# Optimization experiments

Measured on AMD Instinct MI355X. Metric: run time of the kernel, lower is better.

## Reference

```python
import jax, jax.numpy as jnp
import numpy as np

B, N, D = 8, 4096, 1024
NC, NU = 8, 32            # core / universal experts (num_experts=16, occ_factor=1/4)
E = NC + NU               # 40 total experts
S = 2                     # slots per expert
HC, HU = 4 * D, D         # core hidden = 4*dim, occ hidden = 4*occ_factor*dim = dim
L2_EPS = 1e-6
LN_EPS = 1e-5


def l2norm(x):
    n = jnp.sqrt(jnp.sum(x * x, axis=-1, keepdims=True))
    return x * (1.0 / (n + L2_EPS))


def layernorm(x, g, b):
    mu = jnp.mean(x, axis=-1, keepdims=True)
    var = jnp.mean((x - mu) ** 2, axis=-1, keepdims=True)
    return (x - mu) / jnp.sqrt(var + LN_EPS) * g + b


def entmax15(z):
    # exact 1.5-entmax over last axis (sorted algorithm, Peters et al. 2019)
    z = z / 2.0
    z = z - jnp.max(z, axis=-1, keepdims=True)
    zs = -jnp.sort(-z, axis=-1)                      # descending
    K = z.shape[-1]
    k = jnp.arange(1, K + 1, dtype=z.dtype)
    mean = jnp.cumsum(zs, axis=-1) / k
    meansq = jnp.cumsum(zs * zs, axis=-1) / k
    ss = k * (meansq - mean * mean)
    delta = jnp.maximum((1.0 - ss) / k, 1e-12)
    tau = mean - jnp.sqrt(delta)
    support = jnp.sum((tau <= zs).astype(jnp.int32), axis=-1, keepdims=True)
    tau_star = jnp.take_along_axis(tau, support - 1, axis=-1)
    return jnp.maximum(z - tau_star, 0.0) ** 2


def setup_inputs() -> dict:
    key = jax.random.key(0)
    ks = jax.random.split(key, 8)
    return {
        "x": jax.random.normal(ks[0], (B, N, D), jnp.float32),
        "attn_weight": jax.random.uniform(ks[1], (B, 128), jnp.float32),
        "phi": jax.random.normal(ks[2], (E, S, D), jnp.float32) * 0.02,
        "key_gamma": jnp.ones((D,), jnp.float32),
        "key_beta": jnp.zeros((D,), jnp.float32),
        "query_gamma": jnp.ones((D,), jnp.float32),
        "query_beta": jnp.zeros((D,), jnp.float32),
        "ln_gamma": jnp.ones((D,), jnp.float32),
        "ln_beta": jnp.zeros((D,), jnp.float32),
        "scale0": jnp.asarray(0.5, jnp.float32),
        "scale1": jnp.asarray(0.5, jnp.float32),
        "core_w1": jax.random.normal(ks[3], (NC, D, HC), jnp.float32) * (D ** -0.5),
        "core_b1": jnp.zeros((NC, HC), jnp.float32),
        "core_w2": jax.random.normal(ks[4], (NC, HC, D), jnp.float32) * (HC ** -0.5),
        "core_b2": jnp.zeros((NC, D), jnp.float32),
        "occ_w1": jax.random.normal(ks[5], (NU, D, HU), jnp.float32) * (D ** -0.5),
        "occ_b1": jnp.zeros((NU, HU), jnp.float32),
        "occ_w2": jax.random.normal(ks[6], (NU, HU, D), jnp.float32) * (HU ** -0.5),
        "occ_b2": jnp.zeros((NU, D), jnp.float32),
    }


def _expert_mlp(s, w1, b1, w2, b2):
    # s: [b, e, s, d]; per-expert 2-layer MLP with exact GELU
    h = jax.nn.gelu(jnp.einsum('besd,edh->besh', s, w1) + b1[None, :, None, :], approximate=False)
    return jnp.einsum('besh,ehd->besd', h, w2) + b2[None, :, None, :]


def reference(x, attn_weight, phi, key_gamma, key_beta, query_gamma, query_beta,
              ln_gamma, ln_beta, scale0, scale1,
              core_w1, core_b1, core_w2, core_b2,
              occ_w1, occ_b1, occ_w2, occ_b2):
    # keys: OffsetScale then l2norm
    k = l2norm(x * key_gamma + key_beta)
    # queries: OffsetScale -> LayerNorm -> l2norm on phi
    q = layernorm(phi * query_gamma + query_beta, ln_gamma, ln_beta)
    q = l2norm(q)
    logits = jnp.einsum('bnd,esd->bnes', k, q)                      # [B,N,E,S]
    core_mask = (jnp.arange(E) < NC)[None, None, :, None]
    adjusted = jnp.where(core_mask, logits, jnp.asarray(-10000.0, logits.dtype))
    dispatch = jax.nn.softmax(adjusted / scale0, axis=2)            # softmax over experts
    combine = entmax15((adjusted / scale1).reshape(B, N, E * S))    # [B,N,E*S]
    slots = jnp.einsum('bnd,bnes->besd', x, dispatch)               # [B,E,S,D]
    core_out = _expert_mlp(slots[:, :NC], core_w1, core_b1, core_w2, core_b2)
    occ_out = _expert_mlp(slots[:, NC:], occ_w1, occ_b1, occ_w2, occ_b2)
    out = jnp.concatenate([core_out, occ_out], axis=1).reshape(B, E * S, D)
    return jnp.einsum('bsd,bns->bnd', out, combine)                 # [B,N,D]
```

## Files before the change

kernel.cpp:

```cpp
#include <hip/hip_runtime.h>
#include <hip/hip_bf16.h>

#define B_ 8
#define N_ 4096
#define D_ 1024

typedef __attribute__((ext_vector_type(8))) short short8_t;
typedef __attribute__((ext_vector_type(4))) float f32x4;

__device__ __forceinline__ unsigned short f2bf(float f) {
    union { float f; unsigned int u; } v; v.f = f;
    unsigned int r = v.u + 0x7FFF + ((v.u >> 16) & 1);
    return (unsigned short)(r >> 16);
}

__global__ __launch_bounds__(64) void k_prep(
    const float* __restrict__ phi, const float* __restrict__ qg, const float* __restrict__ qb,
    const float* __restrict__ lng, const float* __restrict__ lnb,
    const float* __restrict__ kg, const float* __restrict__ kb,
    unsigned short* __restrict__ qkb, float* __restrict__ cj, float* __restrict__ wbuf)
{
    int r = blockIdx.x;
    int lane = threadIdx.x;
    if (r == 16) {
        float cacc = 0.f;
#pragma unroll
        for (int c = 0; c < 16; ++c) {
            int i = c * 64 + lane;
            float g = kg[i], b = kb[i];
            wbuf[i] = g * g;
            wbuf[1024 + i] = 2.0f * g * b;
            cacc += b * b;
        }
#pragma unroll
        for (int m = 32; m; m >>= 1) cacc += __shfl_xor(cacc, m);
        if (lane == 0) wbuf[2048] = cacc;
        return;
    }
    const float* pr = phi + (size_t)r * D_;
    float v[16];
    float s1 = 0.f;
#pragma unroll
    for (int c = 0; c < 16; ++c) {
        int i = c * 64 + lane;
        v[c] = pr[i] * qg[i] + qb[i];
        s1 += v[c];
    }
#pragma unroll
    for (int m = 32; m; m >>= 1) s1 += __shfl_xor(s1, m);
    float mu = s1 * (1.0f / D_);
    float s2 = 0.f;
#pragma unroll
    for (int c = 0; c < 16; ++c) { float dd = v[c] - mu; s2 += dd * dd; }
#pragma unroll
    for (int m = 32; m; m >>= 1) s2 += __shfl_xor(s2, m);
    float var = s2 * (1.0f / D_);
    float inv = 1.0f / sqrtf(var + 1e-5f);
    float u[16];
    float s3 = 0.f;
#pragma unroll
    for (int c = 0; c < 16; ++c) {
        int i = c * 64 + lane;
        u[c] = (v[c] - mu) * inv * lng[i] + lnb[i];
        s3 += u[c] * u[c];
    }
#pragma unroll
    for (int m = 32; m; m >>= 1) s3 += __shfl_xor(s3, m);
    float rn = 1.0f / (sqrtf(s3) + 1e-6f);
    float cacc = 0.f;
#pragma unroll
    for (int c = 0; c < 16; ++c) {
        int i = c * 64 + lane;
        float qv = u[c] * rn;
        qkb[(size_t)r * D_ + i] = f2bf(qv * kg[i]);
        cacc += qv * kb[i];
    }
#pragma unroll
    for (int m = 32; m; m >>= 1) cacc += __shfl_xor(cacc, m);
    if (lane == 0) cj[r] = cacc;
}

__global__ __launch_bounds__(512) void k_fused(
    const float* __restrict__ x, const unsigned short* __restrict__ qkb,
    const float* __restrict__ wbuf, const float* __restrict__ cj,
    const float* __restrict__ s0p,
    float* __restrict__ lgbuf, float* __restrict__ spart)
{
    __shared__ float smem[6336];
    float* wsd  = smem;
    float* part = smem + 2048;
    float* nrmp = smem + 4096;
    float* sums = smem + 4224;
    float* disp = smem + 5312;

    int tid = threadIdx.x;
    int tok0 = blockIdx.x * 64;
    int wv = tid >> 6;
    int lane = tid & 63;
    int wt = wv & 3;
    int kh = wv >> 2;
    int am = lane & 15;
    int kgr = lane >> 4;

    ((float4*)wsd)[tid] = ((const float4*)wbuf)[tid];
    __syncthreads();

    const float* xrow = x + (size_t)(tok0 + wt * 16 + am) * D_ + kh * 512 + kgr * 8;
    const unsigned short* qrow = qkb + (size_t)am * 1024 + kh * 512 + kgr * 8;
    const float* w2row = wsd + kh * 512 + kgr * 8;
    const float* w1row = wsd + 1024 + kh * 512 + kgr * 8;

    f32x4 acc = {0.f, 0.f, 0.f, 0.f};
    float nrm = 0.f;
#pragma unroll 2
    for (int ks = 0; ks < 16; ++ks) {
        int off = ks * 32;
        float4 a0  = *(const float4*)(xrow + off);
        float4 a1  = *(const float4*)(xrow + off + 4);
        float4 w2a = *(const float4*)(w2row + off);
        float4 w2b = *(const float4*)(w2row + off + 4);
        float4 w1a = *(const float4*)(w1row + off);
        float4 w1b = *(const float4*)(w1row + off + 4);
        nrm += (w2a.x * a0.x + w1a.x) * a0.x + (w2a.y * a0.y + w1a.y) * a0.y
             + (w2a.z * a0.z + w1a.z) * a0.z + (w2a.w * a0.w + w1a.w) * a0.w
             + (w2b.x * a1.x + w1b.x) * a1.x + (w2b.y * a1.y + w1b.y) * a1.y
             + (w2b.z * a1.z + w1b.z) * a1.z + (w2b.w * a1.w + w1b.w) * a1.w;
        union { unsigned short u[8]; short8_t s; } ua;
        ua.u[0] = f2bf(a0.x); ua.u[1] = f2bf(a0.y);
        ua.u[2] = f2bf(a0.z); ua.u[3] = f2bf(a0.w);
        ua.u[4] = f2bf(a1.x); ua.u[5] = f2bf(a1.y);
        ua.u[6] = f2bf(a1.z); ua.u[7] = f2bf(a1.w);
        short8_t bv = *(const short8_t*)(qrow + off);
        acc = __builtin_amdgcn_mfma_f32_16x16x32_bf16(ua.s, bv, acc, 0, 0, 0);
    }
    nrm += __shfl_xor(nrm, 16);
    nrm += __shfl_xor(nrm, 32);

#pragma unroll
    for (int r = 0; r < 4; ++r)
        part[(kh * 64 + wt * 16 + kgr * 4 + r) * 16 + am] = acc[r];
    if (kgr == 0) nrmp[kh * 64 + wt * 16 + am] = nrm;
    __syncthreads();

#pragma unroll
    for (int it = 0; it < 3; ++it) {
        int idx = tid + it * 512;
        if (idx < 1088) {
            int t = idx / 17, v = idx - t * 17;
            float sv = (v < 16) ? (part[t * 16 + v] + part[1024 + t * 16 + v])
                                : (nrmp[t] + nrmp[64 + t]);
            sums[idx] = sv;
            lgbuf[(size_t)(tok0 + t) * 20 + v] = sv;
        }
    }
    __syncthreads();

    if (tid < 64) {
        const float* sp = sums + tid * 17;
        float ss = sp[16] + wbuf[2048];
        float rn = 1.0f / (sqrtf(ss) + 1e-6f);
        float inv0 = 1.0f / s0p[0];
        float lg[16];
#pragma unroll
        for (int j = 0; j < 16; ++j) lg[j] = (sp[j] + cj[j]) * rn;
        float dsp[16];
#pragma unroll
        for (int sl = 0; sl < 2; ++sl) {
            float a[8], m = -1e30f;
#pragma unroll
            for (int ee = 0; ee < 8; ++ee) { a[ee] = lg[2 * ee + sl] * inv0; m = fmaxf(m, a[ee]); }
            float den = 0.f;
#pragma unroll
            for (int ee = 0; ee < 8; ++ee) { a[ee] = expf(a[ee] - m); den += a[ee]; }
            float r = 1.0f / den;
#pragma unroll
            for (int ee = 0; ee < 8; ++ee) dsp[2 * ee + sl] = a[ee] * r;
        }
#pragma unroll
        for (int q4i = 0; q4i < 4; ++q4i)
            *(float4*)(&disp[tid * 16 + q4i * 4]) =
                make_float4(dsp[q4i * 4 + 0], dsp[q4i * 4 + 1], dsp[q4i * 4 + 2], dsp[q4i * 4 + 3]);
    }
    __syncthreads();

    int th = tid >> 8;
    int cix = tid & 255;
    const float* xp = x + (size_t)tok0 * D_ + cix * 4;
    float4 acc2[8];
#pragma unroll
    for (int j = 0; j < 8; ++j) { acc2[j].x = 0.f; acc2[j].y = 0.f; acc2[j].z = 0.f; acc2[j].w = 0.f; }
#pragma unroll 8
    for (int n = 0; n < 64; ++n) {
        float4 xv = *(const float4*)(xp + (size_t)n * D_);
        const float4* q4 = (const float4*)(disp + n * 16 + th * 8);
        float4 s0 = q4[0], s1 = q4[1];
        acc2[0].x += s0.x * xv.x; acc2[0].y += s0.x * xv.y; acc2[0].z += s0.x * xv.z; acc2[0].w += s0.x * xv.w;
        acc2[1].x += s0.y * xv.x; acc2[1].y += s0.y * xv.y; acc2[1].z += s0.y * xv.z; acc2[1].w += s0.y * xv.w;
        acc2[2].x += s0.z * xv.x; acc2[2].y += s0.z * xv.y; acc2[2].z += s0.z * xv.z; acc2[2].w += s0.z * xv.w;
        acc2[3].x += s0.w * xv.x; acc2[3].y += s0.w * xv.y; acc2[3].z += s0.w * xv.z; acc2[3].w += s0.w * xv.w;
        acc2[4].x += s1.x * xv.x; acc2[4].y += s1.x * xv.y; acc2[4].z += s1.x * xv.z; acc2[4].w += s1.x * xv.w;
        acc2[5].x += s1.y * xv.x; acc2[5].y += s1.y * xv.y; acc2[5].z += s1.y * xv.z; acc2[5].w += s1.y * xv.w;
        acc2[6].x += s1.z * xv.x; acc2[6].y += s1.z * xv.y; acc2[6].z += s1.z * xv.z; acc2[6].w += s1.z * xv.w;
        acc2[7].x += s1.w * xv.x; acc2[7].y += s1.w * xv.y; acc2[7].z += s1.w * xv.z; acc2[7].w += s1.w * xv.w;
    }
    float* op = spart + ((size_t)blockIdx.x * 16 + th * 8) * 1024 + cix * 4;
#pragma unroll
    for (int j = 0; j < 8; ++j)
        *(float4*)(op + (size_t)j * 1024) = acc2[j];
}

__global__ __launch_bounds__(64) void k_epi(
    const float* __restrict__ lgbuf, const float* __restrict__ cj,
    const float* __restrict__ wbuf, const float* __restrict__ s1p,
    float* __restrict__ combine)
{
    int tok = blockIdx.x * 64 + threadIdx.x;
    const float* lp = lgbuf + (size_t)tok * 20;
    float s[17];
    float4 q0 = *(const float4*)(lp + 0);
    float4 q1 = *(const float4*)(lp + 4);
    float4 q2 = *(const float4*)(lp + 8);
    float4 q3 = *(const float4*)(lp + 12);
    s[0] = q0.x; s[1] = q0.y; s[2] = q0.z; s[3] = q0.w;
    s[4] = q1.x; s[5] = q1.y; s[6] = q1.z; s[7] = q1.w;
    s[8] = q2.x; s[9] = q2.y; s[10] = q2.z; s[11] = q2.w;
    s[12] = q3.x; s[13] = q3.y; s[14] = q3.z; s[15] = q3.w;
    s[16] = lp[16];

    float ss = s[16] + wbuf[2048];
    float rn = 1.0f / (sqrtf(ss) + 1e-6f);
    float inv1h = 0.5f / s1p[0];
    float lg[16];
#pragma unroll
    for (int j = 0; j < 16; ++j) lg[j] = (s[j] + cj[j]) * rn;

    float z[16], zmax = -1e30f;
#pragma unroll
    for (int j = 0; j < 16; ++j) { z[j] = lg[j] * inv1h; zmax = fmaxf(zmax, z[j]); }
#pragma unroll
    for (int j = 0; j < 16; ++j) z[j] -= zmax;
    float zsr[16];
#pragma unroll
    for (int j = 0; j < 16; ++j) zsr[j] = z[j];
#pragma unroll
    for (int rr = 0; rr < 16; ++rr) {
#pragma unroll
        for (int jj = (rr & 1); jj + 1 < 16; jj += 2) {
            float aa = zsr[jj], bb = zsr[jj + 1];
            zsr[jj] = fmaxf(aa, bb);
            zsr[jj + 1] = fminf(aa, bb);
        }
    }
    float cs = 0.f, css = 0.f, tau_star = 0.f;
#pragma unroll
    for (int kk = 1; kk <= 16; ++kk) {
        cs += zsr[kk - 1];
        css += zsr[kk - 1] * zsr[kk - 1];
        float fk = (float)kk;
        float mean = cs / fk, msq = css / fk;
        float ssv = fk * (msq - mean * mean);
        float delta = fmaxf((1.0f - ssv) / fk, 1e-12f);
        float tau = mean - sqrtf(delta);
        tau_star = (tau <= zsr[kk - 1]) ? tau : tau_star;
    }
    float4* cw = (float4*)(combine + (size_t)tok * 16);
#pragma unroll
    for (int q4i = 0; q4i < 4; ++q4i) {
        float4 cv;
        float t0 = fmaxf(z[q4i * 4 + 0] - tau_star, 0.f);
        float t1 = fmaxf(z[q4i * 4 + 1] - tau_star, 0.f);
        float t2 = fmaxf(z[q4i * 4 + 2] - tau_star, 0.f);
        float t3 = fmaxf(z[q4i * 4 + 3] - tau_star, 0.f);
        cv.x = t0 * t0; cv.y = t1 * t1; cv.z = t2 * t2; cv.w = t3 * t3;
        cw[q4i] = cv;
    }
}

__global__ __launch_bounds__(256) void k_slots_reduce(
    const float* __restrict__ spart, float* __restrict__ slotsT)
{
    int j = blockIdx.x, b = blockIdx.y;
    int tid = threadIdx.x;
    const float* p = spart + ((size_t)(b * 64) * 16 + j) * 1024 + tid * 4;
    float4 s; s.x = 0.f; s.y = 0.f; s.z = 0.f; s.w = 0.f;
#pragma unroll 8
    for (int nc = 0; nc < 64; ++nc) {
        float4 v = *(const float4*)(p + (size_t)nc * 16384);
        s.x += v.x; s.y += v.y; s.z += v.z; s.w += v.w;
    }
    int e = j >> 1, sl = j & 1;
    int t = b * 2 + sl;
    float* o = slotsT + ((size_t)e * 1024 + tid * 4) * 16 + t;
    o[0] = s.x; o[16] = s.y; o[32] = s.z; o[48] = s.w;
}

__global__ __launch_bounds__(256) void k_mlp1(
    const float* __restrict__ w1, const float* __restrict__ slotsT,
    float* __restrict__ p1)
{
    __shared__ float sm[1024];
    int cc = blockIdx.x, ks = blockIdx.y, e = blockIdx.z;
    int tid = threadIdx.x;
    int k0 = ks * 64;
    int col = cc * 1024 + tid * 4;
    ((float4*)sm)[tid] = ((const float4*)(slotsT + ((size_t)e * 1024 + k0) * 16))[tid];
    __syncthreads();

    const float* wp = w1 + (size_t)e * 1024 * 4096 + (size_t)k0 * 4096 + col;
    float4 acc[16];
#pragma unroll
    for (int t = 0; t < 16; ++t) { acc[t].x = 0.f; acc[t].y = 0.f; acc[t].z = 0.f; acc[t].w = 0.f; }
#pragma unroll 8
    for (int kk = 0; kk < 64; ++kk) {
        float4 w = *(const float4*)(wp + (size_t)kk * 4096);
        const float4* q4 = (const float4*)(sm + kk * 16);
        float4 s0 = q4[0], s1 = q4[1], s2 = q4[2], s3 = q4[3];
        acc[0].x  += s0.x * w.x; acc[0].y  += s0.x * w.y; acc[0].z  += s0.x * w.z; acc[0].w  += s0.x * w.w;
        acc[1].x  += s0.y * w.x; acc[1].y  += s0.y * w.y; acc[1].z  += s0.y * w.z; acc[1].w  += s0.y * w.w;
        acc[2].x  += s0.z * w.x; acc[2].y  += s0.z * w.y; acc[2].z  += s0.z * w.z; acc[2].w  += s0.z * w.w;
        acc[3].x  += s0.w * w.x; acc[3].y  += s0.w * w.y; acc[3].z  += s0.w * w.z; acc[3].w  += s0.w * w.w;
        acc[4].x  += s1.x * w.x; acc[4].y  += s1.x * w.y; acc[4].z  += s1.x * w.z; acc[4].w  += s1.x * w.w;
        acc[5].x  += s1.y * w.x; acc[5].y  += s1.y * w.y; acc[5].z  += s1.y * w.z; acc[5].w  += s1.y * w.w;
        acc[6].x  += s1.z * w.x; acc[6].y  += s1.z * w.y; acc[6].z  += s1.z * w.z; acc[6].w  += s1.z * w.w;
        acc[7].x  += s1.w * w.x; acc[7].y  += s1.w * w.y; acc[7].z  += s1.w * w.z; acc[7].w  += s1.w * w.w;
        acc[8].x  += s2.x * w.x; acc[8].y  += s2.x * w.y; acc[8].z  += s2.x * w.z; acc[8].w  += s2.x * w.w;
        acc[9].x  += s2.y * w.x; acc[9].y  += s2.y * w.y; acc[9].z  += s2.y * w.z; acc[9].w  += s2.y * w.w;
        acc[10].x += s2.z * w.x; acc[10].y += s2.z * w.y; acc[10].z += s2.z * w.z; acc[10].w += s2.z * w.w;
        acc[11].x += s2.w * w.x; acc[11].y += s2.w * w.y; acc[11].z += s2.w * w.z; acc[11].w += s2.w * w.w;
        acc[12].x += s3.x * w.x; acc[12].y += s3.x * w.y; acc[12].z += s3.x * w.z; acc[12].w += s3.x * w.w;
        acc[13].x += s3.y * w.x; acc[13].y += s3.y * w.y; acc[13].z += s3.y * w.z; acc[13].w += s3.y * w.w;
        acc[14].x += s3.z * w.x; acc[14].y += s3.z * w.y; acc[14].z += s3.z * w.z; acc[14].w += s3.z * w.w;
        acc[15].x += s3.w * w.x; acc[15].y += s3.w * w.y; acc[15].z += s3.w * w.z; acc[15].w += s3.w * w.w;
    }
    float av0[16], av1[16], av2[16], av3[16];
#pragma unroll
    for (int t = 0; t < 16; ++t) { av0[t] = acc[t].x; av1[t] = acc[t].y; av2[t] = acc[t].z; av3[t] = acc[t].w; }
    float* op = p1 + (((size_t)ks * 8 + e) * 4096 + col) * 16;
#pragma unroll
    for (int q = 0; q < 4; ++q) {
        *(float4*)(op + 0 * 16 + q * 4) = make_float4(av0[q*4+0], av0[q*4+1], av0[q*4+2], av0[q*4+3]);
        *(float4*)(op + 1 * 16 + q * 4) = make_float4(av1[q*4+0], av1[q*4+1], av1[q*4+2], av1[q*4+3]);
        *(float4*)(op + 2 * 16 + q * 4) = make_float4(av2[q*4+0], av2[q*4+1], av2[q*4+2], av2[q*4+3]);
        *(float4*)(op + 3 * 16 + q * 4) = make_float4(av3[q*4+0], av3[q*4+1], av3[q*4+2], av3[q*4+3]);
    }
}

__global__ __launch_bounds__(256) void k_mlp2f(
    const float* __restrict__ w2, const float* __restrict__ p1,
    const float* __restrict__ b1, float* __restrict__ p2)
{
    __shared__ float sm[1024];
    int ks = blockIdx.x, e = blockIdx.y;
    int tid = threadIdx.x;
    int k0 = ks * 64;
    int col = tid * 4;

    {
        int fidx = tid;
        const float* pp = p1 + (size_t)e * 65536 + (size_t)k0 * 16 + fidx * 4;
        float4 s; s.x = 0.f; s.y = 0.f; s.z = 0.f; s.w = 0.f;
#pragma unroll
        for (int ksp = 0; ksp < 16; ++ksp) {
            float4 v = *(const float4*)(pp + (size_t)ksp * 524288);
            s.x += v.x; s.y += v.y; s.z += v.z; s.w += v.w;
        }
        int colh = k0 + (fidx >> 2);
        float bb = b1[(size_t)e * 4096 + colh];
        s.x += bb; s.y += bb; s.z += bb; s.w += bb;
        s.x = 0.5f * s.x * (1.0f + erff(s.x * 0.70710678118654752f));
        s.y = 0.5f * s.y * (1.0f + erff(s.y * 0.70710678118654752f));
        s.z = 0.5f * s.z * (1.0f + erff(s.z * 0.70710678118654752f));
        s.w = 0.5f * s.w * (1.0f + erff(s.w * 0.70710678118654752f));
        *(float4*)(&sm[fidx * 4]) = s;
    }
    __syncthreads();

    const float* wp = w2 + (size_t)e * 4096 * 1024 + (size_t)k0 * 1024 + col;
    float4 acc[16];
#pragma unroll
    for (int t = 0; t < 16; ++t) { acc[t].x = 0.f; acc[t].y = 0.f; acc[t].z = 0.f; acc[t].w = 0.f; }
#pragma unroll 8
    for (int kk = 0; kk < 64; ++kk) {
        float4 w = *(const float4*)(wp + (size_t)kk * 1024);
        const float4* q4 = (const float4*)(sm + kk * 16);
        float4 s0 = q4[0], s1 = q4[1], s2 = q4[2], s3 = q4[3];
        acc[0].x  += s0.x * w.x; acc[0].y  += s0.x * w.y; acc[0].z  += s0.x * w.z; acc[0].w  += s0.x * w.w;
        acc[1].x  += s0.y * w.x; acc[1].y  += s0.y * w.y; acc[1].z  += s0.y * w.z; acc[1].w  += s0.y * w.w;
        acc[2].x  += s0.z * w.x; acc[2].y  += s0.z * w.y; acc[2].z  += s0.z * w.z; acc[2].w  += s0.z * w.w;
        acc[3].x  += s0.w * w.x; acc[3].y  += s0.w * w.y; acc[3].z  += s0.w * w.z; acc[3].w  += s0.w * w.w;
        acc[4].x  += s1.x * w.x; acc[4].y  += s1.x * w.y; acc[4].z  += s1.x * w.z; acc[4].w  += s1.x * w.w;
        acc[5].x  += s1.y * w.x; acc[5].y  += s1.y * w.y; acc[5].z  += s1.y * w.z; acc[5].w  += s1.y * w.w;
        acc[6].x  += s1.z * w.x; acc[6].y  += s1.z * w.y; acc[6].z  += s1.z * w.z; acc[6].w  += s1.z * w.w;
        acc[7].x  += s1.w * w.x; acc[7].y  += s1.w * w.y; acc[7].z  += s1.w * w.z; acc[7].w  += s1.w * w.w;
        acc[8].x  += s2.x * w.x; acc[8].y  += s2.x * w.y; acc[8].z  += s2.x * w.z; acc[8].w  += s2.x * w.w;
        acc[9].x  += s2.y * w.x; acc[9].y  += s2.y * w.y; acc[9].z  += s2.y * w.z; acc[9].w  += s2.y * w.w;
        acc[10].x += s2.z * w.x; acc[10].y += s2.z * w.y; acc[10].z += s2.z * w.z; acc[10].w += s2.z * w.w;
        acc[11].x += s2.w * w.x; acc[11].y += s2.w * w.y; acc[11].z += s2.w * w.z; acc[11].w += s2.w * w.w;
        acc[12].x += s3.x * w.x; acc[12].y += s3.x * w.y; acc[12].z += s3.x * w.z; acc[12].w += s3.x * w.w;
        acc[13].x += s3.y * w.x; acc[13].y += s3.y * w.y; acc[13].z += s3.y * w.z; acc[13].w += s3.y * w.w;
        acc[14].x += s3.z * w.x; acc[14].y += s3.z * w.y; acc[14].z += s3.z * w.z; acc[14].w += s3.z * w.w;
        acc[15].x += s3.w * w.x; acc[15].y += s3.w * w.y; acc[15].z += s3.w * w.z; acc[15].w += s3.w * w.w;
    }
    float av0[16], av1[16], av2[16], av3[16];
#pragma unroll
    for (int t = 0; t < 16; ++t) { av0[t] = acc[t].x; av1[t] = acc[t].y; av2[t] = acc[t].z; av3[t] = acc[t].w; }
    float* op = p2 + (((size_t)ks * 8 + e) * 1024 + col) * 16;
#pragma unroll
    for (int q = 0; q < 4; ++q) {
        *(float4*)(op + 0 * 16 + q * 4) = make_float4(av0[q*4+0], av0[q*4+1], av0[q*4+2], av0[q*4+3]);
        *(float4*)(op + 1 * 16 + q * 4) = make_float4(av1[q*4+0], av1[q*4+1], av1[q*4+2], av1[q*4+3]);
        *(float4*)(op + 2 * 16 + q * 4) = make_float4(av2[q*4+0], av2[q*4+1], av2[q*4+2], av2[q*4+3]);
        *(float4*)(op + 3 * 16 + q * 4) = make_float4(av3[q*4+0], av3[q*4+1], av3[q*4+2], av3[q*4+3]);
    }
}

__global__ __launch_bounds__(256) void k_red2(
    const float* __restrict__ p2, const float* __restrict__ b2,
    float* __restrict__ co)
{
    int idx = blockIdx.x * 256 + threadIdx.x;
    int q = idx & 3, d = (idx >> 2) & 1023, e = idx >> 12;
    const float* p = p2 + ((size_t)e * 1024 + d) * 16 + q * 4;
    float4 s; s.x = 0.f; s.y = 0.f; s.z = 0.f; s.w = 0.f;
#pragma unroll 8
    for (int ks = 0; ks < 64; ++ks) {
        float4 v = *(const float4*)(p + (size_t)ks * 131072);
        s.x += v.x; s.y += v.y; s.z += v.z; s.w += v.w;
    }
    float bb = b2[(size_t)e * 1024 + d];
    float vv[4] = { s.x + bb, s.y + bb, s.z + bb, s.w + bb };
#pragma unroll
    for (int u = 0; u < 4; ++u) {
        int t = q * 4 + u;
        int b = t >> 1, sl = t & 1;
        co[((size_t)b * 16 + e * 2 + sl) * 1024 + d] = vv[u];
    }
}

__global__ __launch_bounds__(256) void k_out(
    const float* __restrict__ co, const float* __restrict__ combine,
    float* __restrict__ out)
{
    __shared__ float sm[1024];
    int b = blockIdx.y, tile = blockIdx.x;
    int tid = threadIdx.x;
    ((float4*)sm)[tid] = ((const float4*)(combine + ((size_t)b * N_ + tile * 64) * 16))[tid];
    float4 cv[16];
#pragma unroll
    for (int j = 0; j < 16; ++j)
        cv[j] = ((const float4*)(co + ((size_t)b * 16 + j) * 1024))[tid];
    __syncthreads();
    float4* ob = (float4*)(out + ((size_t)b * N_ + tile * 64) * 1024) + tid;
#pragma unroll 2
    for (int it = 0; it < 64; ++it) {
        const float* cm = sm + it * 16;
        float4 acc; acc.x = 0.f; acc.y = 0.f; acc.z = 0.f; acc.w = 0.f;
#pragma unroll
        for (int j = 0; j < 16; ++j) {
            float wj = cm[j];
            acc.x += wj * cv[j].x; acc.y += wj * cv[j].y;
            acc.z += wj * cv[j].z; acc.w += wj * cv[j].w;
        }
        ob[(size_t)it * 256] = acc;
    }
}

extern "C" void kernel_launch(void* const* d_in, const int* in_sizes, int n_in,
                              void* d_out, int out_size, void* d_ws, size_t ws_size,
                              hipStream_t stream)
{
    const float* x   = (const float*)d_in[0];
    const float* phi = (const float*)d_in[2];
    const float* kg  = (const float*)d_in[3];
    const float* kb  = (const float*)d_in[4];
    const float* qg  = (const float*)d_in[5];
    const float* qb  = (const float*)d_in[6];
    const float* lng = (const float*)d_in[7];
    const float* lnb = (const float*)d_in[8];
    const float* s0  = (const float*)d_in[9];
    const float* s1  = (const float*)d_in[10];
    const float* w1  = (const float*)d_in[11];
    const float* b1  = (const float*)d_in[12];
    const float* w2  = (const float*)d_in[13];
    const float* b2  = (const float*)d_in[14];

    float* out = (float*)d_out;
    float* ws  = (float*)d_ws;

    unsigned short* qkb = (unsigned short*)ws;
    float* cj       = ws + 8192;
    float* wbuf     = cj + 16;
    float* combine  = wbuf + 2064;
    float* slotsT   = combine + 524288;
    float* co       = slotsT + 131072;
    float* lgbuf    = co + 131072;
    float* arenaA   = lgbuf + 655360;
    float* arenaB   = arenaA + 8388608;
    float* spart    = arenaA;
    float* p1       = arenaA;
    float* p2       = arenaB;

    k_prep        <<<dim3(17),        dim3(64),  0, stream>>>(phi, qg, qb, lng, lnb, kg, kb, qkb, cj, wbuf);
    k_fused       <<<dim3(512),       dim3(512), 0, stream>>>(x, qkb, wbuf, cj, s0, lgbuf, spart);
    k_epi         <<<dim3(512),       dim3(64),  0, stream>>>(lgbuf, cj, wbuf, s1, combine);
    k_slots_reduce<<<dim3(16, 8),     dim3(256), 0, stream>>>(spart, slotsT);
    k_mlp1        <<<dim3(4, 16, 8),  dim3(256), 0, stream>>>(w1, slotsT, p1);
    k_mlp2f       <<<dim3(64, 8),     dim3(256), 0, stream>>>(w2, p1, b1, p2);
    k_red2        <<<dim3(128),       dim3(256), 0, stream>>>(p2, b2, co);
    k_out         <<<dim3(64, 8),     dim3(256), 0, stream>>>(co, combine, out);
}
```

Baseline: 207.1 us.

## Split fused logits/slot kernel into separate logits and slot-accumulation kernels

The fused kernel is split in two. The first computes logits and the dispatch softmax with 256 threads, each wave covering the full K range, which removes the cross-half partial reduction in shared memory. Dispatch weights go to a global buffer, and a second kernel rereads x and dispatch to accumulate slot partials, each thread now holding all 16 slot accumulators. This removes a sync and the split-K reduction, and lowers register and LDS pressure per kernel. The cost is a second full read of x (128 MB) from memory or L2, plus an extra launch.

```diff
diff --git a/kernel.cpp b/kernel.cpp
--- a/kernel.cpp
+++ b/kernel.cpp
@@ -80,40 +80,36 @@
     if (lane == 0) cj[r] = cacc;
 }
 
-__global__ __launch_bounds__(512) void k_fused(
+__global__ __launch_bounds__(256) void k_logits(
     const float* __restrict__ x, const unsigned short* __restrict__ qkb,
     const float* __restrict__ wbuf, const float* __restrict__ cj,
     const float* __restrict__ s0p,
-    float* __restrict__ lgbuf, float* __restrict__ spart)
-{
-    __shared__ float smem[6336];
+    float* __restrict__ lgbuf, float* __restrict__ dispatch)
+{
+    __shared__ float smem[3136];
     float* wsd  = smem;
-    float* part = smem + 2048;
-    float* nrmp = smem + 4096;
-    float* sums = smem + 4224;
-    float* disp = smem + 5312;
+    float* sums = smem + 2048;
 
     int tid = threadIdx.x;
     int tok0 = blockIdx.x * 64;
     int wv = tid >> 6;
     int lane = tid & 63;
-    int wt = wv & 3;
-    int kh = wv >> 2;
     int am = lane & 15;
     int kgr = lane >> 4;
 
     ((float4*)wsd)[tid] = ((const float4*)wbuf)[tid];
+    ((float4*)wsd)[tid + 256] = ((const float4*)wbuf)[tid + 256];
     __syncthreads();
 
-    const float* xrow = x + (size_t)(tok0 + wt * 16 + am) * D_ + kh * 512 + kgr * 8;
-    const unsigned short* qrow = qkb + (size_t)am * 1024 + kh * 512 + kgr * 8;
-    const float* w2row = wsd + kh * 512 + kgr * 8;
-    const float* w1row = wsd + 1024 + kh * 512 + kgr * 8;
+    const float* xrow = x + (size_t)(tok0 + wv * 16 + am) * D_ + kgr * 8;
+    const unsigned short* qrow = qkb + (size_t)am * 1024 + kgr * 8;
+    const float* w2row = wsd + kgr * 8;
+    const float* w1row = wsd + 1024 + kgr * 8;
 
     f32x4 acc = {0.f, 0.f, 0.f, 0.f};
     float nrm = 0.f;
 #pragma unroll 2
-    for (int ks = 0; ks < 16; ++ks) {
+    for (int ks = 0; ks < 32; ++ks) {
         int off = ks * 32;
         float4 a0  = *(const float4*)(xrow + off);
         float4 a1  = *(const float4*)(xrow + off + 4);
@@ -138,22 +134,18 @@
 
 #pragma unroll
     for (int r = 0; r < 4; ++r)
-        part[(kh * 64 + wt * 16 + kgr * 4 + r) * 16 + am] = acc[r];
-    if (kgr == 0) nrmp[kh * 64 + wt * 16 + am] = nrm;
+        sums[(wv * 16 + kgr * 4 + r) * 17 + am] = acc[r];
+    if (kgr == 0) sums[(wv * 16 + am) * 17 + 16] = nrm;
     __syncthreads();
 
 #pragma unroll
-    for (int it = 0; it < 3; ++it) {
-        int idx = tid + it * 512;
+    for (int it = 0; it < 5; ++it) {
+        int idx = tid + it * 256;
         if (idx < 1088) {
             int t = idx / 17, v = idx - t * 17;
-            float sv = (v < 16) ? (part[t * 16 + v] + part[1024 + t * 16 + v])
-                                : (nrmp[t] + nrmp[64 + t]);
-            sums[idx] = sv;
-            lgbuf[(size_t)(tok0 + t) * 20 + v] = sv;
+            lgbuf[(size_t)(tok0 + t) * 20 + v] = sums[idx];
         }
     }
-    __syncthreads();
 
     if (tid < 64) {
         const float* sp = sums + tid * 17;
@@ -176,36 +168,53 @@
 #pragma unroll
             for (int ee = 0; ee < 8; ++ee) dsp[2 * ee + sl] = a[ee] * r;
         }
+        float4* dw = (float4*)(dispatch + (size_t)(tok0 + tid) * 16);
 #pragma unroll
         for (int q4i = 0; q4i < 4; ++q4i)
-            *(float4*)(&disp[tid * 16 + q4i * 4]) =
-                make_float4(dsp[q4i * 4 + 0], dsp[q4i * 4 + 1], dsp[q4i * 4 + 2], dsp[q4i * 4 + 3]);
-    }
+            dw[q4i] = make_float4(dsp[q4i * 4 + 0], dsp[q4i * 4 + 1],
+                                  dsp[q4i * 4 + 2], dsp[q4i * 4 + 3]);
+    }
+}
+
+__global__ __launch_bounds__(256) void k_spart(
+    const float* __restrict__ x, const float* __restrict__ dispatch,
+    float* __restrict__ spart)
+{
+    __shared__ float disp[1024];
+    int tid = threadIdx.x;
+    int tok0 = blockIdx.x * 64;
+    ((float4*)disp)[tid] = ((const float4*)(dispatch + (size_t)tok0 * 16))[tid];
     __syncthreads();
 
-    int th = tid >> 8;
-    int cix = tid & 255;
-    const float* xp = x + (size_t)tok0 * D_ + cix * 4;
-    float4 acc2[8];
-#pragma unroll
-    for (int j = 0; j < 8; ++j) { acc2[j].x = 0.f; acc2[j].y = 0.f; acc2[j].z = 0.f; acc2[j].w = 0.f; }
-#pragma unroll 8
+    const float* xp = x + (size_t)tok0 * D_ + tid * 4;
+    float4 acc2[16];
+#pragma unroll
+    for (int j = 0; j < 16; ++j) { acc2[j].x = 0.f; acc2[j].y = 0.f; acc2[j].z = 0.f; acc2[j].w = 0.f; }
+#pragma unroll 4
     for (int n = 0; n < 64; ++n) {
         float4 xv = *(const float4*)(xp + (size_t)n * D_);
-        const float4* q4 = (const float4*)(disp + n * 16 + th * 8);
-        float4 s0 = q4[0], s1 = q4[1];
-        acc2[0].x += s0.x * xv.x; acc2[0].y += s0.x * xv.y; acc2[0].z += s0.x * xv.z; acc2[0].w += s0.x * xv.w;
-        acc2[1].x += s0.y * xv.x; acc2[1].y += s0.y * xv.y; acc2[1].z += s0.y * xv.z; acc2[1].w += s0.y * xv.w;
-        acc2[2].x += s0.z * xv.x; acc2[2].y += s0.z * xv.y; acc2[2].z += s0.z * xv.z; acc2[2].w += s0.z * xv.w;
-        acc2[3].x += s0.w * xv.x; acc2[3].y += s0.w * xv.y; acc2[3].z += s0.w * xv.z; acc2[3].w += s0.w * xv.w;
-        acc2[4].x += s1.x * xv.x; acc2[4].y += s1.x * xv.y; acc2[4].z += s1.x * xv.z; acc2[4].w += s1.x * xv.w;
-        acc2[5].x += s1.y * xv.x; acc2[5].y += s1.y * xv.y; acc2[5].z += s1.y * xv.z; acc2[5].w += s1.y * xv.w;
-        acc2[6].x += s1.z * xv.x; acc2[6].y += s1.z * xv.y; acc2[6].z += s1.z * xv.z; acc2[6].w += s1.z * xv.w;
-        acc2[7].x += s1.w * xv.x; acc2[7].y += s1.w * xv.y; acc2[7].z += s1.w * xv.z; acc2[7].w += s1.w * xv.w;
-    }
-    float* op = spart + ((size_t)blockIdx.x * 16 + th * 8) * 1024 + cix * 4;
-#pragma unroll
-    for (int j = 0; j < 8; ++j)
+        const float4* q4 = (const float4*)(disp + n * 16);
+        float4 s0 = q4[0], s1 = q4[1], s2 = q4[2], s3 = q4[3];
+        acc2[0].x  += s0.x * xv.x; acc2[0].y  += s0.x * xv.y; acc2[0].z  += s0.x * xv.z; acc2[0].w  += s0.x * xv.w;
+        acc2[1].x  += s0.y * xv.x; acc2[1].y  += s0.y * xv.y; acc2[1].z  += s0.y * xv.z; acc2[1].w  += s0.y * xv.w;
+        acc2[2].x  += s0.z * xv.x; acc2[2].y  += s0.z * xv.y; acc2[2].z  += s0.z * xv.z; acc2[2].w  += s0.z * xv.w;
+        acc2[3].x  += s0.w * xv.x; acc2[3].y  += s0.w * xv.y; acc2[3].z  += s0.w * xv.z; acc2[3].w  += s0.w * xv.w;
+        acc2[4].x  += s1.x * xv.x; acc2[4].y  += s1.x * xv.y; acc2[4].z  += s1.x * xv.z; acc2[4].w  += s1.x * xv.w;
+        acc2[5].x  += s1.y * xv.x; acc2[5].y  += s1.y * xv.y; acc2[5].z  += s1.y * xv.z; acc2[5].w  += s1.y * xv.w;
+        acc2[6].x  += s1.z * xv.x; acc2[6].y  += s1.z * xv.y; acc2[6].z  += s1.z * xv.z; acc2[6].w  += s1.z * xv.w;
+        acc2[7].x  += s1.w * xv.x; acc2[7].y  += s1.w * xv.y; acc2[7].z  += s1.w * xv.z; acc2[7].w  += s1.w * xv.w;
+        acc2[8].x  += s2.x * xv.x; acc2[8].y  += s2.x * xv.y; acc2[8].z  += s2.x * xv.z; acc2[8].w  += s2.x * xv.w;
+        acc2[9].x  += s2.y * xv.x; acc2[9].y  += s2.y * xv.y; acc2[9].z  += s2.y * xv.z; acc2[9].w  += s2.y * xv.w;
+        acc2[10].x += s2.z * xv.x; acc2[10].y += s2.z * xv.y; acc2[10].z += s2.z * xv.z; acc2[10].w += s2.z * xv.w;
+        acc2[11].x += s2.w * xv.x; acc2[11].y += s2.w * xv.y; acc2[11].z += s2.w * xv.z; acc2[11].w += s2.w * xv.w;
+        acc2[12].x += s3.x * xv.x; acc2[12].y += s3.x * xv.y; acc2[12].z += s3.x * xv.z; acc2[12].w += s3.x * xv.w;
+        acc2[13].x += s3.y * xv.x; acc2[13].y += s3.y * xv.y; acc2[13].z += s3.y * xv.z; acc2[13].w += s3.y * xv.w;
+        acc2[14].x += s3.z * xv.x; acc2[14].y += s3.z * xv.y; acc2[14].z += s3.z * xv.z; acc2[14].w += s3.z * xv.w;
+        acc2[15].x += s3.w * xv.x; acc2[15].y += s3.w * xv.y; acc2[15].z += s3.w * xv.z; acc2[15].w += s3.w * xv.w;
+    }
+    float* op = spart + ((size_t)blockIdx.x * 16) * 1024 + tid * 4;
+#pragma unroll
+    for (int j = 0; j < 16; ++j)
         *(float4*)(op + (size_t)j * 1024) = acc2[j];
 }
 
@@ -491,7 +500,8 @@
     float* cj       = ws + 8192;
     float* wbuf     = cj + 16;
     float* combine  = wbuf + 2064;
-    float* slotsT   = combine + 524288;
+    float* dispatch = combine + 524288;
+    float* slotsT   = dispatch + 524288;
     float* co       = slotsT + 131072;
     float* lgbuf    = co + 131072;
     float* arenaA   = lgbuf + 655360;
@@ -501,7 +511,8 @@
     float* p2       = arenaB;
 
     k_prep        <<<dim3(17),        dim3(64),  0, stream>>>(phi, qg, qb, lng, lnb, kg, kb, qkb, cj, wbuf);
-    k_fused       <<<dim3(512),       dim3(512), 0, stream>>>(x, qkb, wbuf, cj, s0, lgbuf, spart);
+    k_logits      <<<dim3(512),       dim3(256), 0, stream>>>(x, qkb, wbuf, cj, s0, lgbuf, dispatch);
+    k_spart       <<<dim3(512),       dim3(256), 0, stream>>>(x, dispatch, spart);
     k_epi         <<<dim3(512),       dim3(64),  0, stream>>>(lgbuf, cj, wbuf, s1, combine);
     k_slots_reduce<<<dim3(16, 8),     dim3(256), 0, stream>>>(spart, slotsT);
     k_mlp1        <<<dim3(4, 16, 8),  dim3(256), 0, stream>>>(w1, slotsT, p1);
```

Result: slower. 227.1 us (+9.7%).
